# Kernel optimization log

Measured on AMD Instinct MI355X. Metric: run time of the kernel, lower is better.

The kernel has to match this reference:

```python
import jax, jax.numpy as jnp
import numpy as np

PAD = 0  # padding_index
BIG = 10000.0

B, S = 1024, 128
V, E, H, T = 200, 512, 512, 24


def setup_inputs() -> dict:
    key = jax.random.key(0)
    ks = jax.random.split(key, 12)
    sequences = jax.random.randint(ks[0], (B, S), 0, V, dtype=jnp.int32)
    labels = jax.random.randint(ks[1], (B, S), 0, T, dtype=jnp.int32)
    true_lengths = jax.random.randint(ks[2], (B,), 1, S, dtype=jnp.int32)
    emb = jax.random.normal(ks[3], (V, E), dtype=jnp.float32) * 0.1
    emb = emb.at[PAD].set(0.0)  # nn.Embedding padding_idx zeros that row
    w1 = jax.random.normal(ks[4], (H, H), dtype=jnp.float32) * (1.0 / np.sqrt(H))
    b1 = jax.random.normal(ks[5], (H,), dtype=jnp.float32) * 0.01
    w2 = jax.random.normal(ks[6], (T, H), dtype=jnp.float32) * (1.0 / np.sqrt(H))
    b2 = jax.random.normal(ks[7], (T,), dtype=jnp.float32) * 0.01
    start_trans = jax.random.uniform(ks[8], (T,), jnp.float32, -0.1, 0.1)
    end_trans = jax.random.uniform(ks[9], (T,), jnp.float32, -0.1, 0.1)
    transitions = jax.random.uniform(ks[10], (T, T), jnp.float32, -0.1, 0.1)
    return {"sequences": sequences, "labels": labels, "true_lengths": true_lengths,
            "emb": emb, "w1": w1, "b1": b1, "w2": w2, "b2": b2,
            "start_trans": start_trans, "end_trans": end_trans, "transitions": transitions}


def _emissions(sequences, emb, w1, b1, w2, b2):
    pad_mask = (sequences == PAD).astype(jnp.float32)  # [B,S]
    x = emb[sequences]                                  # [B,S,E]
    h = jax.nn.relu(x @ w1.T + b1)                      # [B,S,H]
    scores = jax.nn.relu(h @ w2.T + b2)                 # [B,S,T]
    scores = scores.at[:, :, PAD].add(pad_mask * BIG)
    return scores


def _crf_nll_mean(emissions, labels, start_trans, end_trans, transitions):
    # emissions [B,S,T], labels [B,S]; mask = all ones (none passed in forward)
    # numerator: score of gold path
    em_gold = jnp.take_along_axis(emissions, labels[..., None], axis=2)[..., 0]  # [B,S]
    num = (start_trans[labels[:, 0]]
           + em_gold.sum(axis=1)
           + transitions[labels[:, :-1], labels[:, 1:]].sum(axis=1)
           + end_trans[labels[:, -1]])  # [B]
    # denominator: forward algorithm via scan over time
    em_t = jnp.swapaxes(emissions, 0, 1)  # [S,B,T]
    alpha0 = start_trans[None, :] + em_t[0]  # [B,T]

    def step(alpha, emit):
        # alpha [B,T_prev], transitions [T_prev,T_next], emit [B,T_next]
        nxt = jax.nn.logsumexp(alpha[:, :, None] + transitions[None] + emit[:, None, :], axis=1)
        return nxt, None

    alpha, _ = jax.lax.scan(step, alpha0, em_t[1:])
    denom = jax.nn.logsumexp(alpha + end_trans[None, :], axis=1)  # [B]
    llh = num - denom
    return -jnp.mean(llh)


def reference(sequences, labels, true_lengths, emb, w1, b1, w2, b2,
              start_trans, end_trans, transitions):
    emissions = _emissions(sequences, emb, w1, b1, w2, b2)
    return _crf_nll_mean(emissions, labels, start_trans, end_trans, transitions)
```

## Files before the change

kernel.cpp:

```cpp
#include <hip/hip_runtime.h>
#include <math.h>

#define PAD_IDX 0
#define BIGV 10000.0f
constexpr int B_ = 1024, S_ = 128, V_ = 200, E_ = 512, H_ = 512, T_ = 24;

constexpr int OFF_H  = 262144;
constexpr int OFF_EM = 364544;
constexpr int OFF_W  = 369344;
constexpr int OFF_MX = 374144;

typedef __attribute__((ext_vector_type(8)))  short    bf8frag;
typedef __attribute__((ext_vector_type(16))) float    facc16;
typedef __attribute__((ext_vector_type(4)))  unsigned u32x4;

__device__ __forceinline__ unsigned short f2bf(float f) {
    unsigned u = __float_as_uint(f);
    u += 0x7fffu + ((u >> 16) & 1u);
    return (unsigned short)(u >> 16);
}
__device__ __forceinline__ unsigned pkbf(float lo, float hi) {
    const unsigned a = __float_as_uint(lo), b = __float_as_uint(hi);
    return ((a + 0x8000u) >> 16) | ((b + 0x8000u) & 0xffff0000u);
}

__global__ __launch_bounds__(256) void transpose_kernel(
    const float* __restrict__ w1, unsigned short* __restrict__ w1Tb,
    float* __restrict__ out)
{
    __shared__ float tile[64][65];
    const int bi = blockIdx.x >> 3, bj = blockIdx.x & 7;
    const int tx = threadIdx.x & 63, r0 = (threadIdx.x >> 6) * 16;
    if (blockIdx.x == 0 && threadIdx.x == 0) out[0] = 0.f;
    #pragma unroll
    for (int m = 0; m < 16; ++m) {
        const int r = r0 + m;
        tile[r][tx] = w1[(size_t)(bi * 64 + r) * 512 + bj * 64 + tx];
    }
    __syncthreads();
    #pragma unroll
    for (int m = 0; m < 16; ++m) {
        const int r = r0 + m;
        w1Tb[(size_t)(bj * 64 + r) * 512 + bi * 64 + tx] = f2bf(tile[tx][r]);
    }
}

__global__ __launch_bounds__(256) void h_kernel(
    const float* __restrict__ emb, const unsigned short* __restrict__ w1Tb,
    const float* __restrict__ b1, float* __restrict__ h_ws)
{
    __shared__ float xi[2 * E_];
    __shared__ float part_s[4][64][8];
    const int pair = blockIdx.x >> 1, half = blockIdx.x & 1;
    const int v0 = pair * 2, v1 = v0 + 1;
    const int tid = threadIdx.x;
    {
        const float* __restrict__ x0 = emb + (size_t)v0 * E_;
        const float* __restrict__ x1 = emb + (size_t)v1 * E_;
        #pragma unroll
        for (int m = 0; m < 2; ++m) {
            const int k = tid + m * 256;
            xi[2 * k]     = x0[k];
            xi[2 * k + 1] = x1[k];
        }
    }
    __syncthreads();
    const int part = tid >> 6, quad = tid & 63;
    const int t0 = half * 256 + quad * 4, k0 = part * 128;
    float a0 = 0.f, a1 = 0.f, a2 = 0.f, a3 = 0.f;
    float c0 = 0.f, c1 = 0.f, c2 = 0.f, c3 = 0.f;
    const unsigned short* __restrict__ wp = w1Tb + (size_t)k0 * H_ + t0;
    const float2* __restrict__ xp = (const float2*)xi + k0;
    #pragma unroll 4
    for (int i = 0; i < 128; ++i) {
        const uint2 wu = *(const uint2*)(wp + (size_t)i * H_);
        const float2 x = xp[i];
        const float w0 = __uint_as_float(wu.x << 16);
        const float w1v = __uint_as_float(wu.x & 0xffff0000u);
        const float w2v = __uint_as_float(wu.y << 16);
        const float w3v = __uint_as_float(wu.y & 0xffff0000u);
        a0 = fmaf(w0,  x.x, a0); a1 = fmaf(w1v, x.x, a1);
        a2 = fmaf(w2v, x.x, a2); a3 = fmaf(w3v, x.x, a3);
        c0 = fmaf(w0,  x.y, c0); c1 = fmaf(w1v, x.y, c1);
        c2 = fmaf(w2v, x.y, c2); c3 = fmaf(w3v, x.y, c3);
    }
    part_s[part][quad][0] = a0; part_s[part][quad][1] = a1;
    part_s[part][quad][2] = a2; part_s[part][quad][3] = a3;
    part_s[part][quad][4] = c0; part_s[part][quad][5] = c1;
    part_s[part][quad][6] = c2; part_s[part][quad][7] = c3;
    __syncthreads();
    {
        const int q2 = tid >> 2, r0 = tid & 3;
        const float s0 = (part_s[0][q2][r0]     + part_s[1][q2][r0])
                       + (part_s[2][q2][r0]     + part_s[3][q2][r0]);
        const float s1 = (part_s[0][q2][r0 + 4] + part_s[1][q2][r0 + 4])
                       + (part_s[2][q2][r0 + 4] + part_s[3][q2][r0 + 4]);
        const int t = half * 256 + tid;
        const float bb = b1[t];
        h_ws[(size_t)v0 * H_ + t] = fmaxf(s0 + bb, 0.f);
        h_ws[(size_t)v1 * H_ + t] = fmaxf(s1 + bb, 0.f);
    }
}

__global__ __launch_bounds__(256) void emis_kernel(
    const float* __restrict__ h_ws, const float* __restrict__ w2,
    const float* __restrict__ b2, float* __restrict__ em_table,
    float* __restrict__ w_table, float* __restrict__ emax_arr)
{
    __shared__ float em_row[32];
    const int v = blockIdx.x;
    const int t = threadIdx.x;
    const int wave = t >> 6, lane = t & 63;
    const float* __restrict__ hrow = h_ws + (size_t)v * H_;
    for (int jj2 = 0; jj2 < 6; ++jj2) {
        const int jo = wave * 6 + jj2;
        float part = 0.f;
        #pragma unroll
        for (int m = 0; m < H_ / 64; ++m) {
            const int k = lane + m * 64;
            part = fmaf(hrow[k], w2[(size_t)jo * H_ + k], part);
        }
        #pragma unroll
        for (int off = 32; off; off >>= 1)
            part += __shfl_xor(part, off, 64);
        if (lane == 0) {
            float val = fmaxf(part + b2[jo], 0.f);
            if (v == 0 && jo == PAD_IDX) val += BIGV;
            em_row[jo] = val;
        }
    }
    __syncthreads();
    if (t < 32) {
        float x = (t < T_) ? em_row[t] : -INFINITY;
        float mx = x;
        #pragma unroll
        for (int off = 16; off; off >>= 1)
            mx = fmaxf(mx, __shfl_xor(mx, off, 32));
        if (t < T_) {
            em_table[v * T_ + t] = x;
            w_table[v * T_ + t]  = __expf(x - mx);
        }
        if (t == 0) emax_arr[v] = mx;
    }
}

__global__ __launch_bounds__(256) void crf_kernel(
    const int* __restrict__ seq, const int* __restrict__ labels,
    const float* __restrict__ start_t, const float* __restrict__ end_t,
    const float* __restrict__ trans, const float* __restrict__ em_table,
    const float* __restrict__ w_table, const float* __restrict__ emax_arr,
    float* __restrict__ out)
{
    __shared__ __align__(16) float w_s[V_ * T_];
    __shared__ int   tok_s[S_ * 32];
    __shared__ float meet_s[64 * 12];
    __shared__ float logb_s[64];
    __shared__ float gp_s[32];
    const int tid = threadIdx.x;
    const int g = blockIdx.x;

    for (int i = tid; i < V_ * T_ / 4; i += 256)
        ((float4*)w_s)[i] = ((const float4*)w_table)[i];
    {
        const int bq = tid & 31, c = tid >> 5;
        const int* __restrict__ src = seq + (size_t)(g * 32 + bq) * S_ + c * 16;
        #pragma unroll
        for (int i = 0; i < 16; ++i)
            tok_s[(c * 16 + i) * 32 + bq] = src[i];
    }
    if (tid < 32) gp_s[tid] = 0.f;
    __syncthreads();

    if (tid < 128) {
        const bool isF = (tid < 64);
        const int lane = tid & 63;
        const int n = lane & 31;
        const int h = lane >> 5;

        u32x4 A1p, A2p;
        {
            float a1e[8], a2e[8];
            #pragma unroll
            for (int j = 0; j < 8; ++j) {
                const int k1 = 8 * h + j;
                const int k2 = 16 + 8 * h + j;
                float v1 = 0.f, v2 = 0.f;
                if (n < T_) {
                    v1 = __expf(isF ? trans[k1 * T_ + n] : trans[n * T_ + k1]);
                    if (k2 < T_)
                        v2 = __expf(isF ? trans[k2 * T_ + n] : trans[n * T_ + k2]);
                }
                a1e[j] = v1; a2e[j] = v2;
            }
            #pragma unroll
            for (int r = 0; r < 4; ++r) {
                A1p[r] = pkbf(a1e[2 * r], a1e[2 * r + 1]);
                A2p[r] = pkbf(a2e[2 * r], a2e[2 * r + 1]);
            }
        }

        float logacc;
        u32x4 B1p, B2p;
        {
            const int tokI = tok_s[(isF ? 0 : (S_ - 1)) * 32 + n];
            float q1[8], q2[8];
            if (isF) {
                float e1[8], e2[8];
                #pragma unroll
                for (int j = 0; j < 8; ++j) { e1[j] = 0.f; e2[j] = 0.f; }
                float mx = -INFINITY;
                #pragma unroll
                for (int j = 0; j < 8; ++j) {
                    const int r1 = 8 * h + j;
                    e1[j] = start_t[r1] + em_table[tokI * T_ + r1];
                    mx = fmaxf(mx, e1[j]);
                }
                if (h == 0) {
                    #pragma unroll
                    for (int j = 0; j < 8; ++j) {
                        const int r2 = 16 + j;
                        e2[j] = start_t[r2] + em_table[tokI * T_ + r2];
                        mx = fmaxf(mx, e2[j]);
                    }
                }
                mx = fmaxf(mx, __shfl_xor(mx, 32, 64));
                #pragma unroll
                for (int j = 0; j < 8; ++j) {
                    q1[j] = __expf(e1[j] - mx);
                    q2[j] = (h == 0) ? __expf(e2[j] - mx) : 0.f;
                }
                logacc = mx;
            } else {
                #pragma unroll
                for (int j = 0; j < 8; ++j) {
                    const int r1 = 8 * h + j;
                    q1[j] = w_s[tokI * T_ + r1] * __expf(end_t[r1]);
                    const int r2 = 16 + j;
                    q2[j] = (h == 0) ? w_s[tokI * T_ + r2] * __expf(end_t[r2]) : 0.f;
                }
                logacc = 0.f;
            }
            #pragma unroll
            for (int r = 0; r < 4; ++r) {
                B1p[r] = pkbf(q1[2 * r], q1[2 * r + 1]);
                B2p[r] = pkbf(q2[2 * r], q2[2 * r + 1]);
            }
        }

        const int dir  = isF ? 1 : -1;
        const int offi = isF ? 1 : (S_ - 2);

        float4 Wc0, Wc1, Wc2;
        {
            const int tk = tok_s[offi * 32 + n];
            const float* wb = w_s + tk * T_ + 4 * h;
            Wc0 = *(const float4*)(wb);
            Wc1 = *(const float4*)(wb + 8);
            Wc2 = *(const float4*)(wb + 16);
        }

        float d[12];
        for (int s = 1; s <= 63; ++s) {
            const int sn = (s < 63) ? (s + 1) : 63;
            const int tkN = tok_s[(offi + dir * (sn - 1)) * 32 + n];
            const float* wbn = w_s + tkN * T_ + 4 * h;
            const float4 Wn0 = *(const float4*)(wbn);
            const float4 Wn1 = *(const float4*)(wbn + 8);
            const float4 Wn2 = *(const float4*)(wbn + 16);

            facc16 accA, accB;
            #pragma unroll
            for (int r = 0; r < 16; ++r) { accA[r] = 0.f; accB[r] = 0.f; }
            accA = __builtin_amdgcn_mfma_f32_32x32x16_bf16(
                       __builtin_bit_cast(bf8frag, A1p),
                       __builtin_bit_cast(bf8frag, B1p), accA, 0, 0, 0);
            accB = __builtin_amdgcn_mfma_f32_32x32x16_bf16(
                       __builtin_bit_cast(bf8frag, A2p),
                       __builtin_bit_cast(bf8frag, B2p), accB, 0, 0, 0);

            d[0]  = (accA[0]  + accB[0] ) * Wc0.x;
            d[1]  = (accA[1]  + accB[1] ) * Wc0.y;
            d[2]  = (accA[2]  + accB[2] ) * Wc0.z;
            d[3]  = (accA[3]  + accB[3] ) * Wc0.w;
            d[4]  = (accA[4]  + accB[4] ) * Wc1.x;
            d[5]  = (accA[5]  + accB[5] ) * Wc1.y;
            d[6]  = (accA[6]  + accB[6] ) * Wc1.z;
            d[7]  = (accA[7]  + accB[7] ) * Wc1.w;
            d[8]  = (accA[8]  + accB[8] ) * Wc2.x;
            d[9]  = (accA[9]  + accB[9] ) * Wc2.y;
            d[10] = (accA[10] + accB[10]) * Wc2.z;
            d[11] = (accA[11] + accB[11]) * Wc2.w;

            if ((s & 15) == 0 || s == 63) {
                float mx = d[0];
                #pragma unroll
                for (int r = 1; r < 12; ++r) mx = fmaxf(mx, d[r]);
                mx = fmaxf(mx, __shfl_xor(mx, 32, 64));
                const float inv = 1.0f / mx;
                #pragma unroll
                for (int r = 0; r < 12; ++r) d[r] *= inv;
                logacc += __logf(mx);
            }

            const unsigned P0 = pkbf(d[0], d[1]),  P1 = pkbf(d[2], d[3]);
            const unsigned P2 = pkbf(d[4], d[5]),  P3 = pkbf(d[6], d[7]);
            const unsigned P4 = pkbf(d[8], d[9]),  P5 = pkbf(d[10], d[11]);
            const unsigned XP0 = (unsigned)__shfl_xor((int)P0, 32, 64);
            const unsigned XP1 = (unsigned)__shfl_xor((int)P1, 32, 64);
            const unsigned XP2 = (unsigned)__shfl_xor((int)P2, 32, 64);
            const unsigned XP3 = (unsigned)__shfl_xor((int)P3, 32, 64);
            const unsigned XP4 = (unsigned)__shfl_xor((int)P4, 32, 64);
            const unsigned XP5 = (unsigned)__shfl_xor((int)P5, 32, 64);
            B1p[0] = h ? XP2 : P0;  B1p[1] = h ? XP3 : P1;
            B1p[2] = h ? P2  : XP0; B1p[3] = h ? P3  : XP1;
            B2p[0] = h ? 0u  : P4;  B2p[1] = h ? 0u  : P5;
            B2p[2] = h ? 0u  : XP4; B2p[3] = h ? 0u  : XP5;

            Wc0 = Wn0; Wc1 = Wn1; Wc2 = Wn2;
        }

        if (!isF) {
            #pragma unroll
            for (int r = 0; r < 12; ++r) meet_s[lane * 12 + r] = d[r];
            logb_s[lane] = logacc;
        }
        __syncthreads();
        if (isF) {
            facc16 accA, accB;
            #pragma unroll
            for (int r = 0; r < 16; ++r) { accA[r] = 0.f; accB[r] = 0.f; }
            accA = __builtin_amdgcn_mfma_f32_32x32x16_bf16(
                       __builtin_bit_cast(bf8frag, A1p),
                       __builtin_bit_cast(bf8frag, B1p), accA, 0, 0, 0);
            accB = __builtin_amdgcn_mfma_f32_32x32x16_bf16(
                       __builtin_bit_cast(bf8frag, A2p),
                       __builtin_bit_cast(bf8frag, B2p), accB, 0, 0, 0);
            float dot = 0.f;
            #pragma unroll
            for (int r = 0; r < 12; ++r)
                dot = fmaf(accA[r] + accB[r], meet_s[lane * 12 + r], dot);
            dot += __shfl_xor(dot, 32, 64);
            const float denom = logacc + logb_s[lane] + __logf(dot);
            float val = 0.f;
            if (h == 0)
                val = (denom - gp_s[n]) * (1.0f / (float)B_);
            #pragma unroll
            for (int off = 32; off; off >>= 1)
                val += __shfl_xor(val, off, 64);
            if (lane == 0) atomicAdd(out, val);
        }
    } else {
        const int t2 = tid - 128;
        const int n = t2 & 31;
        const int r = t2 >> 5;
        const int b = g * 32 + n;
        const int* __restrict__ lrow = labels + (size_t)b * S_;
        float gp = 0.f;
        for (int i = 0; i < 32; ++i) {
            const int s = r * 32 + i;
            const int tk = tok_s[s * 32 + n];
            const int ls = lrow[s];
            gp += em_table[tk * T_ + ls];
            if (s >= 1) gp -= emax_arr[tk];
            if (s < S_ - 1) gp += trans[ls * T_ + lrow[s + 1]];
            if (s == 0) gp += start_t[ls];
            if (s == S_ - 1) gp += end_t[ls];
        }
        atomicAdd(&gp_s[n], gp);
        __syncthreads();
    }
}

extern "C" void kernel_launch(void* const* d_in, const int* in_sizes, int n_in,
                              void* d_out, int out_size, void* d_ws, size_t ws_size,
                              hipStream_t stream) {
    const int*   seq     = (const int*)d_in[0];
    const int*   labels  = (const int*)d_in[1];
    const float* emb     = (const float*)d_in[3];
    const float* w1      = (const float*)d_in[4];
    const float* b1      = (const float*)d_in[5];
    const float* w2      = (const float*)d_in[6];
    const float* b2      = (const float*)d_in[7];
    const float* start_t = (const float*)d_in[8];
    const float* end_t   = (const float*)d_in[9];
    const float* trans   = (const float*)d_in[10];

    float* ws            = (float*)d_ws;
    unsigned short* w1Tb = (unsigned short*)d_ws;
    float* h_ws          = ws + OFF_H;
    float* em_table      = ws + OFF_EM;
    float* w_table       = ws + OFF_W;
    float* emax_arr      = ws + OFF_MX;
    float* out           = (float*)d_out;

    transpose_kernel<<<64, 256, 0, stream>>>(w1, w1Tb, out);
    h_kernel<<<200, 256, 0, stream>>>(emb, w1Tb, b1, h_ws);
    emis_kernel<<<V_, 256, 0, stream>>>(h_ws, w2, b2, em_table, w_table, emax_arr);
    crf_kernel<<<B_ / 32, 256, 0, stream>>>(seq, labels, start_t, end_t, trans,
                                            em_table, w_table, emax_arr, out);
}
```

Measured before the change: 117.6 us.

## Fuse W1 transpose and hidden-layer GEMV into one MFMA tiled kernel

Replaces the separate W1 transpose-to-bf16 kernel and the scalar-FMA hidden-layer kernel with one kernel. Each block loads a 32x32 tile of vocab rows and hidden units, packs both operands to bf16 in shared memory, and computes the 200x512 product with 32x32x16 bf16 MFMA, splitting K across four waves and reducing through shared memory. This drops one kernel launch and the intermediate transposed weight buffer. In exchange, emb and W1 are both rounded to bf16 and each block reloads full 512-wide rows.

Result: faster. 108.9 us, median of 2 (-7.3%).

```diff
diff --git a/kernel.cpp b/kernel.cpp
--- a/kernel.cpp
+++ b/kernel.cpp
@@ -14,91 +14,96 @@
 typedef __attribute__((ext_vector_type(16))) float    facc16;
 typedef __attribute__((ext_vector_type(4)))  unsigned u32x4;
 
-__device__ __forceinline__ unsigned short f2bf(float f) {
-    unsigned u = __float_as_uint(f);
-    u += 0x7fffu + ((u >> 16) & 1u);
-    return (unsigned short)(u >> 16);
-}
 __device__ __forceinline__ unsigned pkbf(float lo, float hi) {
     const unsigned a = __float_as_uint(lo), b = __float_as_uint(hi);
     return ((a + 0x8000u) >> 16) | ((b + 0x8000u) & 0xffff0000u);
 }
 
-__global__ __launch_bounds__(256) void transpose_kernel(
-    const float* __restrict__ w1, unsigned short* __restrict__ w1Tb,
+__global__ __launch_bounds__(256) void mlp1_kernel(
+    const float* __restrict__ emb, const float* __restrict__ w1,
+    const float* __restrict__ b1, float* __restrict__ h_ws,
     float* __restrict__ out)
 {
-    __shared__ float tile[64][65];
-    const int bi = blockIdx.x >> 3, bj = blockIdx.x & 7;
-    const int tx = threadIdx.x & 63, r0 = (threadIdx.x >> 6) * 16;
-    if (blockIdx.x == 0 && threadIdx.x == 0) out[0] = 0.f;
-    #pragma unroll
-    for (int m = 0; m < 16; ++m) {
-        const int r = r0 + m;
-        tile[r][tx] = w1[(size_t)(bi * 64 + r) * 512 + bj * 64 + tx];
+    __shared__ unsigned w1b[256][32];
+    __shared__ unsigned embb[256][32];
+    __shared__ float    part[4][64][17];
+    const int tid = threadIdx.x;
+    const int vt = blockIdx.x % 7, tt = blockIdx.x / 7;
+    const int v0 = vt * 32, t0 = tt * 32;
+
+    if (blockIdx.x == 0 && tid == 0) out[0] = 0.f;
+
+    {
+        const int row = tid >> 3;
+        const int seg = tid & 7;
+        {
+            const float* __restrict__ src = w1 + (size_t)(t0 + row) * E_ + seg * 64;
+            #pragma unroll
+            for (int i = 0; i < 16; ++i) {
+                const float4 f = *(const float4*)(src + i * 4);
+                const int kp = seg * 32 + i * 2;
+                w1b[kp][row]     = pkbf(f.x, f.y);
+                w1b[kp + 1][row] = pkbf(f.z, f.w);
+            }
+        }
+        const int v = v0 + row;
+        if (v < V_) {
+            const float* __restrict__ src = emb + (size_t)v * E_ + seg * 64;
+            #pragma unroll
+            for (int i = 0; i < 16; ++i) {
+                const float4 f = *(const float4*)(src + i * 4);
+                const int kp = seg * 32 + i * 2;
+                embb[kp][row]     = pkbf(f.x, f.y);
+                embb[kp + 1][row] = pkbf(f.z, f.w);
+            }
+        } else {
+            #pragma unroll
+            for (int i = 0; i < 16; ++i) {
+                const int kp = seg * 32 + i * 2;
+                embb[kp][row] = 0u; embb[kp + 1][row] = 0u;
+            }
+        }
     }
     __syncthreads();
-    #pragma unroll
-    for (int m = 0; m < 16; ++m) {
-        const int r = r0 + m;
-        w1Tb[(size_t)(bj * 64 + r) * 512 + bi * 64 + tx] = f2bf(tile[tx][r]);
-    }
-}
-
-__global__ __launch_bounds__(256) void h_kernel(
-    const float* __restrict__ emb, const unsigned short* __restrict__ w1Tb,
-    const float* __restrict__ b1, float* __restrict__ h_ws)
-{
-    __shared__ float xi[2 * E_];
-    __shared__ float part_s[4][64][8];
-    const int pair = blockIdx.x >> 1, half = blockIdx.x & 1;
-    const int v0 = pair * 2, v1 = v0 + 1;
-    const int tid = threadIdx.x;
+
     {
-        const float* __restrict__ x0 = emb + (size_t)v0 * E_;
-        const float* __restrict__ x1 = emb + (size_t)v1 * E_;
-        #pragma unroll
-        for (int m = 0; m < 2; ++m) {
-            const int k = tid + m * 256;
-            xi[2 * k]     = x0[k];
-            xi[2 * k + 1] = x1[k];
-        }
+        const int wave = tid >> 6, lane = tid & 63;
+        const int mn = lane & 31, h2 = lane >> 5;
+        facc16 acc;
+        #pragma unroll
+        for (int r = 0; r < 16; ++r) acc[r] = 0.f;
+        #pragma unroll
+        for (int c = 0; c < 8; ++c) {
+            const int kp = wave * 64 + c * 8 + 4 * h2;
+            u32x4 Af, Bf;
+            #pragma unroll
+            for (int r = 0; r < 4; ++r) {
+                Af[r] = embb[kp + r][mn];
+                Bf[r] = w1b[kp + r][mn];
+            }
+            acc = __builtin_amdgcn_mfma_f32_32x32x16_bf16(
+                      __builtin_bit_cast(bf8frag, Af),
+                      __builtin_bit_cast(bf8frag, Bf), acc, 0, 0, 0);
+        }
+        #pragma unroll
+        for (int r = 0; r < 16; ++r) part[wave][lane][r] = acc[r];
     }
     __syncthreads();
-    const int part = tid >> 6, quad = tid & 63;
-    const int t0 = half * 256 + quad * 4, k0 = part * 128;
-    float a0 = 0.f, a1 = 0.f, a2 = 0.f, a3 = 0.f;
-    float c0 = 0.f, c1 = 0.f, c2 = 0.f, c3 = 0.f;
-    const unsigned short* __restrict__ wp = w1Tb + (size_t)k0 * H_ + t0;
-    const float2* __restrict__ xp = (const float2*)xi + k0;
-    #pragma unroll 4
-    for (int i = 0; i < 128; ++i) {
-        const uint2 wu = *(const uint2*)(wp + (size_t)i * H_);
-        const float2 x = xp[i];
-        const float w0 = __uint_as_float(wu.x << 16);
-        const float w1v = __uint_as_float(wu.x & 0xffff0000u);
-        const float w2v = __uint_as_float(wu.y << 16);
-        const float w3v = __uint_as_float(wu.y & 0xffff0000u);
-        a0 = fmaf(w0,  x.x, a0); a1 = fmaf(w1v, x.x, a1);
-        a2 = fmaf(w2v, x.x, a2); a3 = fmaf(w3v, x.x, a3);
-        c0 = fmaf(w0,  x.y, c0); c1 = fmaf(w1v, x.y, c1);
-        c2 = fmaf(w2v, x.y, c2); c3 = fmaf(w3v, x.y, c3);
-    }
-    part_s[part][quad][0] = a0; part_s[part][quad][1] = a1;
-    part_s[part][quad][2] = a2; part_s[part][quad][3] = a3;
-    part_s[part][quad][4] = c0; part_s[part][quad][5] = c1;
-    part_s[part][quad][6] = c2; part_s[part][quad][7] = c3;
-    __syncthreads();
+
     {
-        const int q2 = tid >> 2, r0 = tid & 3;
-        const float s0 = (part_s[0][q2][r0]     + part_s[1][q2][r0])
-                       + (part_s[2][q2][r0]     + part_s[3][q2][r0]);
-        const float s1 = (part_s[0][q2][r0 + 4] + part_s[1][q2][r0 + 4])
-                       + (part_s[2][q2][r0 + 4] + part_s[3][q2][r0 + 4]);
-        const int t = half * 256 + tid;
-        const float bb = b1[t];
-        h_ws[(size_t)v0 * H_ + t] = fmaxf(s0 + bb, 0.f);
-        h_ws[(size_t)v1 * H_ + t] = fmaxf(s1 + bb, 0.f);
+        const int l = tid & 63, rg = tid >> 6;
+        const int col = l & 31, hh = l >> 5;
+        const float bb = b1[t0 + col];
+        #pragma unroll
+        for (int i = 0; i < 4; ++i) {
+            const int r = rg * 4 + i;
+            const float s = (part[0][l][r] + part[1][l][r])
+                          + (part[2][l][r] + part[3][l][r]);
+            const int vrow = (r & 3) + 8 * (r >> 2) + 4 * hh;
+            const int v = v0 + vrow;
+            if (v < V_)
+                h_ws[(size_t)v * H_ + t0 + col] = fmaxf(s + bb, 0.f);
+        }
     }
 }
 
@@ -386,15 +391,13 @@
     const float* trans   = (const float*)d_in[10];
 
     float* ws            = (float*)d_ws;
-    unsigned short* w1Tb = (unsigned short*)d_ws;
     float* h_ws          = ws + OFF_H;
     float* em_table      = ws + OFF_EM;
     float* w_table       = ws + OFF_W;
     float* emax_arr      = ws + OFF_MX;
     float* out           = (float*)d_out;
 
-    transpose_kernel<<<64, 256, 0, stream>>>(w1, w1Tb, out);
-    h_kernel<<<200, 256, 0, stream>>>(emb, w1Tb, b1, h_ws);
+    mlp1_kernel<<<112, 256, 0, stream>>>(emb, w1, b1, h_ws, out);
     emis_kernel<<<V_, 256, 0, stream>>>(h_ws, w2, b2, em_table, w_table, emax_arr);
     crf_kernel<<<B_ / 32, 256, 0, stream>>>(seq, labels, start_t, end_t, trans,
                                             em_table, w_table, emax_arr, out);
```
